# Kernel optimization log

Hardware: AMD Instinct MI355X
Metric: run time of the kernel (lower is better)

The kernel has to match this reference:

```python
import jax, jax.numpy as jnp
import numpy as np

QLEN, BSZ, D_MODEL = 2048, 2, 1024
N_HEAD, D_HEAD = 16, 64
SCALE = 1.0 / (D_HEAD ** 0.5)
LN_EPS = 1e-5


def _rel_shift(x):
    # x: [qlen, klen, bsz, n_head]
    q, k, b, n = x.shape
    zero_pad = jnp.zeros((q, 1, b, n), dtype=x.dtype)
    x_padded = jnp.concatenate([zero_pad, x], axis=1).reshape(k + 1, q, b, n)
    return x_padded[1:].reshape(q, k, b, n)


def setup_inputs() -> dict:
    key = jax.random.key(0)
    ks = jax.random.split(key, 6)
    w = jax.random.normal(ks[0], (QLEN, BSZ, D_MODEL), dtype=jnp.float32)
    r_emb = jax.random.normal(ks[1], (QLEN, N_HEAD, D_HEAD), dtype=jnp.float32) * 0.02
    r_w_bias = jax.random.normal(ks[2], (N_HEAD, D_HEAD), dtype=jnp.float32) * 0.02
    r_bias = jax.random.normal(ks[3], (QLEN, N_HEAD), dtype=jnp.float32) * 0.02
    # causal mask (1 above diagonal => masked), dim==2 branch of original forward
    attn_mask = jnp.triu(jnp.ones((QLEN, QLEN), dtype=jnp.float32), k=1)
    W_qkv = jax.random.normal(ks[4], (D_MODEL, 3 * N_HEAD * D_HEAD), dtype=jnp.float32) * (D_MODEL ** -0.5)
    W_o = jax.random.normal(ks[5], (N_HEAD * D_HEAD, D_MODEL), dtype=jnp.float32) * (D_MODEL ** -0.5)
    ln_g = jnp.ones((D_MODEL,), dtype=jnp.float32)
    ln_b = jnp.zeros((D_MODEL,), dtype=jnp.float32)
    return {"w": w, "r_emb": r_emb, "r_w_bias": r_w_bias, "r_bias": r_bias,
            "attn_mask": attn_mask, "W_qkv": W_qkv, "W_o": W_o, "ln_g": ln_g, "ln_b": ln_b}


def reference(w, r_emb, r_w_bias, r_bias, attn_mask, W_qkv, W_o, ln_g, ln_b):
    qlen, bsz, d_model = w.shape
    n_head, d_head = r_w_bias.shape

    w_heads = w @ W_qkv                                   # [q, b, 3*n*d]
    q_h, k_h, v_h = jnp.split(w_heads, 3, axis=-1)
    q_h = q_h.reshape(qlen, bsz, n_head, d_head)
    k_h = k_h.reshape(qlen, bsz, n_head, d_head)
    v_h = v_h.reshape(qlen, bsz, n_head, d_head)
    klen = k_h.shape[0]

    # klen == r_emb.size(0) here, so slicing is a no-op (kept for fidelity)
    r_emb_s = r_emb[-klen:]
    r_bias_s = r_bias[-klen:]

    rw_head_q = q_h + r_w_bias[None, None]                # [q, b, n, d]
    AC = jnp.einsum('ibnd,jbnd->ijbn', rw_head_q, k_h)    # content-content
    B_ = jnp.einsum('ibnd,jnd->ijbn', q_h, r_emb_s)       # content-position
    D_ = r_bias_s[None, :, None, :]                       # [1, k, 1, n]
    BD = _rel_shift(B_ + D_)

    attn_score = (AC + BD) * SCALE
    attn_score = attn_score + attn_mask[:, :, None, None] * (-1e9)
    attn_prob = jax.nn.softmax(attn_score, axis=1)

    attn_vec = jnp.einsum('ijbn,jbnd->ibnd', attn_prob, v_h)
    attn_vec = attn_vec.reshape(qlen, bsz, n_head * d_head)
    attn_out = attn_vec @ W_o

    # residual + LayerNorm
    y = w + attn_out
    mu = jnp.mean(y, axis=-1, keepdims=True)
    var = jnp.var(y, axis=-1, keepdims=True)
    return (y - mu) / jnp.sqrt(var + LN_EPS) * ln_g + ln_b
```

## Files before the change

kernel.cpp:

```cpp
#include <hip/hip_runtime.h>

typedef unsigned short ushort_t;
typedef unsigned short us4 __attribute__((ext_vector_type(4)));
typedef unsigned short us8 __attribute__((ext_vector_type(8)));
typedef unsigned int   u32x4 __attribute__((ext_vector_type(4)));
typedef float          f32x4 __attribute__((ext_vector_type(4)));
typedef __bf16         bf16x8 __attribute__((ext_vector_type(8)));

#define SCALE2 0.18033688011112042f

__device__ __forceinline__ unsigned short f2bf(float f) {
  unsigned u = __builtin_bit_cast(unsigned, f);
  u += 0x7fffu + ((u >> 16) & 1u);
  return (unsigned short)(u >> 16);
}
__device__ __forceinline__ float bf2f(unsigned short h) {
  unsigned u = ((unsigned)h) << 16;
  return __builtin_bit_cast(float, u);
}

__device__ __forceinline__ float fast_exp2(float x) {
  return __builtin_amdgcn_exp2f(x);
}

__device__ __forceinline__ void async_cp16(const ushort_t* g, ushort_t* l) {
  __builtin_amdgcn_global_load_lds(
      (const __attribute__((address_space(1))) unsigned int*)g,
      (__attribute__((address_space(3))) unsigned int*)l, 16, 0, 0);
}

template <int CTRL>
__device__ __forceinline__ float dpp_rotf(float x) {
  return __builtin_bit_cast(float,
      __builtin_amdgcn_update_dpp(0, __builtin_bit_cast(int, x), CTRL, 0xF, 0xF, true));
}
__device__ __forceinline__ float row16_max(float x) {
  x = fmaxf(x, dpp_rotf<0x121>(x));
  x = fmaxf(x, dpp_rotf<0x122>(x));
  x = fmaxf(x, dpp_rotf<0x124>(x));
  x = fmaxf(x, dpp_rotf<0x128>(x));
  return x;
}
__device__ __forceinline__ float row16_sum(float x) {
  x += dpp_rotf<0x121>(x);
  x += dpp_rotf<0x122>(x);
  x += dpp_rotf<0x124>(x);
  x += dpp_rotf<0x128>(x);
  return x;
}


__global__ __launch_bounds__(256) void k_conv_x(const float* __restrict__ in,
                                                ushort_t* __restrict__ out) {
  int i = (blockIdx.x * 256 + threadIdx.x) * 4;
  float4 v = *(const float4*)(in + i);
  us4 o;
  o[0] = f2bf(v.x); o[1] = f2bf(v.y); o[2] = f2bf(v.z); o[3] = f2bf(v.w);
  *(us4*)(out + i) = o;
}

__global__ __launch_bounds__(256) void k_transpose_bf16(const float* __restrict__ in,
                                                        ushort_t* __restrict__ out,
                                                        int R, int C) {
  __shared__ float tile[32][33];
  int c0 = blockIdx.x * 32, r0 = blockIdx.y * 32;
  int tx = threadIdx.x, ty = threadIdx.y;
#pragma unroll
  for (int k = 0; k < 32; k += 8)
    tile[ty + k][tx] = in[(size_t)(r0 + ty + k) * C + c0 + tx];
  __syncthreads();
#pragma unroll
  for (int k = 0; k < 32; k += 8)
    out[(size_t)(c0 + ty + k) * R + r0 + tx] = f2bf(tile[tx][ty + k]);
}

__global__ __launch_bounds__(256) void k_conv_remb(const float* __restrict__ re,
                                                   ushort_t* __restrict__ out) {
  int tid = blockIdx.x * 256 + threadIdx.x;
  int o = tid * 8;
  int d = o & 63, r = (o >> 6) & 2047, h = o >> 17;
  const float* src = re + ((size_t)r * 16 + h) * 64 + d;
  float4 a = *(const float4*)(src);
  float4 b = *(const float4*)(src + 4);
  us8 u;
  u[0] = f2bf(a.x); u[1] = f2bf(a.y); u[2] = f2bf(a.z); u[3] = f2bf(a.w);
  u[4] = f2bf(b.x); u[5] = f2bf(b.y); u[6] = f2bf(b.z); u[7] = f2bf(b.w);
  *(us8*)(out + o) = u;
}

__global__ __launch_bounds__(256) void k_rbias2(const ushort_t* __restrict__ RE,
                                                const float* __restrict__ rwb,
                                                const float* __restrict__ rbias,
                                                float* __restrict__ out) {
  int tid = blockIdx.x * 256 + threadIdx.x;
  int h = tid >> 11, r = tid & 2047;
  const ushort_t* re = RE + ((size_t)h * 2048 + r) * 64;
  const float* wv = rwb + h * 64;
  float acc = 0.f;
#pragma unroll
  for (int d0 = 0; d0 < 64; d0 += 8) {
    us8 v = *(const us8*)(re + d0);
#pragma unroll
    for (int e = 0; e < 8; ++e) acc += bf2f(v[e]) * wv[d0 + e];
  }
  out[h * 2048 + r] = (rbias[r * 16 + h] - acc) * SCALE2;
}


__global__ __launch_bounds__(256) void k_gemm_qkv(const ushort_t* __restrict__ A,
                                                  const ushort_t* __restrict__ B,
                                                  const float* __restrict__ rwb,
                                                  ushort_t* __restrict__ qt,
                                                  ushort_t* __restrict__ kk,
                                                  ushort_t* __restrict__ vv) {
  __shared__ ushort_t Al[128 * 32], Bl[128 * 32];
  int row0 = blockIdx.x * 128, col0 = blockIdx.y * 128;
  int t = threadIdx.x, w = t >> 6, l = t & 63;
  int wr = w >> 1, wc = w & 1, g = l >> 4, cl = l & 15;
  f32x4 acc[4][4];
#pragma unroll
  for (int m = 0; m < 4; ++m)
#pragma unroll
    for (int n = 0; n < 4; ++n) acc[m][n] = (f32x4){0.f, 0.f, 0.f, 0.f};
  for (int k0 = 0; k0 < 1024; k0 += 32) {
#pragma unroll
    for (int c = 0; c < 2; ++c) {
      int u = t + 256 * c, row = u >> 2, col = (u & 3) * 8;
      async_cp16(A + (size_t)(row0 + row) * 1024 + k0 + col, &Al[u * 8]);
      async_cp16(B + (size_t)(col0 + row) * 1024 + k0 + col, &Bl[u * 8]);
    }
    __syncthreads();
    bf16x8 af[4], bfr[4];
#pragma unroll
    for (int m = 0; m < 4; ++m) af[m] = *(const bf16x8*)(&Al[(wr * 64 + m * 16 + cl) * 32 + g * 8]);
#pragma unroll
    for (int n = 0; n < 4; ++n) bfr[n] = *(const bf16x8*)(&Bl[(wc * 64 + n * 16 + cl) * 32 + g * 8]);
#pragma unroll
    for (int m = 0; m < 4; ++m)
#pragma unroll
      for (int n = 0; n < 4; ++n)
        acc[m][n] = __builtin_amdgcn_mfma_f32_16x16x32_bf16(af[m], bfr[n], acc[m][n], 0, 0, 0);
    __syncthreads();
  }
  int sec = col0 >> 10;
#pragma unroll
  for (int m = 0; m < 4; ++m) {
#pragma unroll
    for (int n = 0; n < 4; ++n) {
#pragma unroll
      for (int r = 0; r < 4; ++r) {
        int row = row0 + wr * 64 + m * 16 + g * 4 + r;
        int col = col0 + wc * 64 + n * 16 + cl;
        int mm = col & 1023, hh = mm >> 6, d = mm & 63;
        int bq = row & 1, iq = row >> 1;
        float val = acc[m][n][r];
        if (sec == 0) {
          qt[(((size_t)bq * 16 + hh) * 2048 + iq) * 64 + d] = f2bf((val + rwb[mm]) * SCALE2);
        } else if (sec == 1) {
          kk[(((size_t)bq * 16 + hh) * 2048 + iq) * 64 + d] = f2bf(val);
        } else {
          vv[(((size_t)bq * 16 + hh) * 64 + d) * 2048 + iq] = f2bf(val);
        }
      }
    }
  }
}


__global__ __launch_bounds__(256, 3) void k_flash(const ushort_t* __restrict__ QT,
                                                  const ushort_t* __restrict__ KK,
                                                  const ushort_t* __restrict__ VT,
                                                  const ushort_t* __restrict__ RE,
                                                  const float* __restrict__ RB2,
                                                  ushort_t* __restrict__ AV) {
  int bh = blockIdx.x, b = bh >> 4, h = bh & 15;
  int i0 = (gridDim.y - 1 - blockIdx.y) * 64;
  int t = threadIdx.x, w = t >> 6, l = t & 63, g = l >> 4, cl = l & 15;

  __shared__ ushort_t Klds[64 * 72];
  __shared__ ushort_t Vt[64 * 72];
  __shared__ ushort_t Rl[128 * 72];
  __shared__ float rb2s[128];
  __shared__ ushort_t Pls[4][16 * 76];
  __shared__ float alphal[4][16];
  __shared__ float lsuml[4][16];

  const ushort_t* qb = QT + ((size_t)(b * 16 + h)) * 2048 * 64;
  const ushort_t* kb = KK + ((size_t)(b * 16 + h)) * 2048 * 64;
  const ushort_t* vt = VT + ((size_t)(b * 16 + h)) * 64 * 2048;
  const ushort_t* rbase = RE + (size_t)h * 2048 * 64;
  const float* r2 = RB2 + h * 2048;

  int qrow = i0 + w * 16 + cl;
  bf16x8 qa0 = *(const bf16x8*)(qb + (size_t)qrow * 64 + g * 8);
  bf16x8 qa1 = *(const bf16x8*)(qb + (size_t)qrow * 64 + 32 + g * 8);

  float m_run[4], l_run[4];
  f32x4 Ot[4];
#pragma unroll
  for (int r = 0; r < 4; ++r) { m_run[r] = -1e30f; l_run[r] = 0.f; }
#pragma unroll
  for (int dt = 0; dt < 4; ++dt) Ot[dt] = (f32x4){0.f, 0.f, 0.f, 0.f};

  int nt = gridDim.y - blockIdx.y;
  int rb0f = 1984 - i0;
  int urow = t >> 3, ucol = (t & 7) * 8;

  *(u32x4*)(&Rl[((rb0f + urow) & 127) * 72 + ucol]) =
      *(const u32x4*)(rbase + (size_t)(rb0f + urow) * 64 + ucol);
  *(u32x4*)(&Rl[((rb0f + urow + 32) & 127) * 72 + ucol]) =
      *(const u32x4*)(rbase + (size_t)(rb0f + urow + 32) * 64 + ucol);
  if (t < 64) rb2s[(rb0f + t) & 127] = r2[rb0f + t];

  u32x4 kreg0, kreg1, vreg0, vreg1, rreg0, rreg1;
  float rb2reg;

  {
    kreg0 = *(const u32x4*)(kb + (size_t)urow * 64 + ucol);
    kreg1 = *(const u32x4*)(kb + (size_t)(urow + 32) * 64 + ucol);
    vreg0 = *(const u32x4*)(vt + (size_t)urow * 2048 + ucol);
    vreg1 = *(const u32x4*)(vt + (size_t)(urow + 32) * 2048 + ucol);
    int gs = rb0f + 64;
    int rr0 = gs + urow, rr1 = gs + urow + 32;
    rreg0 = (rr0 < 2048) ? *(const u32x4*)(rbase + (size_t)rr0 * 64 + ucol) : (u32x4){0u, 0u, 0u, 0u};
    rreg1 = (rr1 < 2048) ? *(const u32x4*)(rbase + (size_t)rr1 * 64 + ucol) : (u32x4){0u, 0u, 0u, 0u};
    int rrb = gs + t;
    rb2reg = (t < 64 && rrb < 2048) ? r2[rrb] : 0.f;
  }

  for (int tt = 0; tt < nt; ++tt) {
    int j0 = tt * 64;
    int rb0 = rb0f + j0;
    __syncthreads();
    {
      *(u32x4*)(&Klds[urow * 72 + ucol]) = kreg0;
      *(u32x4*)(&Klds[(urow + 32) * 72 + ucol]) = kreg1;
      *(u32x4*)(&Vt[urow * 72 + ucol]) = vreg0;
      *(u32x4*)(&Vt[(urow + 32) * 72 + ucol]) = vreg1;
      int gs = rb0 + 64;
      *(u32x4*)(&Rl[((gs + urow) & 127) * 72 + ucol]) = rreg0;
      *(u32x4*)(&Rl[((gs + urow + 32) & 127) * 72 + ucol]) = rreg1;
      if (t < 64) rb2s[(gs + t) & 127] = rb2reg;
    }
    __syncthreads();
    if (tt + 1 < nt) {
      int j0n = j0 + 64;
      kreg0 = *(const u32x4*)(kb + (size_t)(j0n + urow) * 64 + ucol);
      kreg1 = *(const u32x4*)(kb + (size_t)(j0n + urow + 32) * 64 + ucol);
      vreg0 = *(const u32x4*)(vt + (size_t)urow * 2048 + j0n + ucol);
      vreg1 = *(const u32x4*)(vt + (size_t)(urow + 32) * 2048 + j0n + ucol);
      int gs = rb0f + j0n + 64;
      int rr0 = gs + urow, rr1 = gs + urow + 32;
      rreg0 = (rr0 < 2048) ? *(const u32x4*)(rbase + (size_t)rr0 * 64 + ucol) : (u32x4){0u, 0u, 0u, 0u};
      rreg1 = (rr1 < 2048) ? *(const u32x4*)(rbase + (size_t)rr1 * 64 + ucol) : (u32x4){0u, 0u, 0u, 0u};
      int rrb = gs + t;
      rb2reg = (t < 64 && rrb < 2048) ? r2[rrb] : 0.f;
    }

    int bw0 = 48 - 16 * w;
    int rB = rb0 + bw0;
    f32x4 bwf[5];
    __builtin_amdgcn_s_setprio(1);
#pragma unroll
    for (int ct = 0; ct < 5; ++ct) {
      int prow = (rB + ct * 16) & 127;
      f32x4 a = (f32x4){0.f, 0.f, 0.f, 0.f};
      bf16x8 rr0 = *(const bf16x8*)(&Rl[(prow + cl) * 72 + g * 8]);
      a = __builtin_amdgcn_mfma_f32_16x16x32_bf16(qa0, rr0, a, 0, 0, 0);
      bf16x8 rr1 = *(const bf16x8*)(&Rl[(prow + cl) * 72 + 32 + g * 8]);
      a = __builtin_amdgcn_mfma_f32_16x16x32_bf16(qa1, rr1, a, 0, 0, 0);
      float rv = rb2s[(prow + cl) & 127];
      a[0] += rv; a[1] += rv; a[2] += rv; a[3] += rv;
      bwf[ct] = a;
    }

    f32x4 S[4];
#pragma unroll
    for (int ct = 0; ct < 4; ++ct) {
      f32x4 a = (f32x4){0.f, 0.f, 0.f, 0.f};
      bf16x8 kf0 = *(const bf16x8*)(&Klds[(ct * 16 + cl) * 72 + g * 8]);
      a = __builtin_amdgcn_mfma_f32_16x16x32_bf16(qa0, kf0, a, 0, 0, 0);
      bf16x8 kf1 = *(const bf16x8*)(&Klds[(ct * 16 + cl) * 72 + 32 + g * 8]);
      a = __builtin_amdgcn_mfma_f32_16x16x32_bf16(qa1, kf1, a, 0, 0, 0);
      S[ct] = a;
    }
    __builtin_amdgcn_s_setprio(0);

    bool diag = (tt == nt - 1);
    int climit = i0 - j0 + 15 + 16 * w;
#pragma unroll
    for (int r = 0; r < 4; ++r) {
      int rl = g * 4 + r;
      int dlt = cl - rl + 15;
      int src = (l & 48) | (dlt & 15);
      float b0 = __shfl(bwf[0][r], src);
      float b1 = __shfl(bwf[1][r], src);
      float b2 = __shfl(bwf[2][r], src);
      float b3 = __shfl(bwf[3][r], src);
      float b4 = __shfl(bwf[4][r], src);
      if (dlt >= 16) { b0 = b1; b1 = b2; b2 = b3; b3 = b4; }
      float sv[4];
      if (diag) {
        sv[0] = (dlt      <= climit) ? S[0][r] + b0 : -1e30f;
        sv[1] = (dlt + 16 <= climit) ? S[1][r] + b1 : -1e30f;
        sv[2] = (dlt + 32 <= climit) ? S[2][r] + b2 : -1e30f;
        sv[3] = (dlt + 48 <= climit) ? S[3][r] + b3 : -1e30f;
      } else {
        sv[0] = S[0][r] + b0;
        sv[1] = S[1][r] + b1;
        sv[2] = S[2][r] + b2;
        sv[3] = S[3][r] + b3;
      }
      float rmax = fmaxf(fmaxf(sv[0], sv[1]), fmaxf(sv[2], sv[3]));
      rmax = row16_max(rmax);
      float mn = fmaxf(m_run[r], rmax);
      float al = fast_exp2(m_run[r] - mn);
      m_run[r] = mn;
      float rsum = 0.f;
#pragma unroll
      for (int ct = 0; ct < 4; ++ct) {
        float pv = fast_exp2(sv[ct] - mn);
        sv[ct] = pv;
        rsum += pv;
      }
      rsum = row16_sum(rsum);
      l_run[r] = l_run[r] * al + rsum;
      if (cl == 0) alphal[w][rl] = al;
#pragma unroll
      for (int ct = 0; ct < 4; ++ct)
        Pls[w][rl * 76 + ct * 16 + cl] = f2bf(sv[ct]);
    }

    float aq = alphal[w][cl];
    bf16x8 pb0 = *(const bf16x8*)(&Pls[w][cl * 76 + g * 8]);
    bf16x8 pb1 = *(const bf16x8*)(&Pls[w][cl * 76 + 32 + g * 8]);
    __builtin_amdgcn_s_setprio(1);
#pragma unroll
    for (int dt = 0; dt < 4; ++dt) {
      f32x4 o = Ot[dt];
      o[0] *= aq; o[1] *= aq; o[2] *= aq; o[3] *= aq;
      bf16x8 va0 = *(const bf16x8*)(&Vt[(dt * 16 + cl) * 72 + g * 8]);
      o = __builtin_amdgcn_mfma_f32_16x16x32_bf16(va0, pb0, o, 0, 0, 0);
      bf16x8 va1 = *(const bf16x8*)(&Vt[(dt * 16 + cl) * 72 + 32 + g * 8]);
      o = __builtin_amdgcn_mfma_f32_16x16x32_bf16(va1, pb1, o, 0, 0, 0);
      Ot[dt] = o;
    }
    __builtin_amdgcn_s_setprio(0);
  }

  if (cl == 0) {
#pragma unroll
    for (int r = 0; r < 4; ++r) lsuml[w][g * 4 + r] = l_run[r];
  }
  float inv = 1.f / lsuml[w][cl];
  int orow = (i0 + w * 16 + cl) * 2 + b;
#pragma unroll
  for (int dt = 0; dt < 4; ++dt) {
    us4 o4;
    o4[0] = f2bf(Ot[dt][0] * inv);
    o4[1] = f2bf(Ot[dt][1] * inv);
    o4[2] = f2bf(Ot[dt][2] * inv);
    o4[3] = f2bf(Ot[dt][3] * inv);
    *(us4*)(&AV[(size_t)orow * 1024 + h * 64 + dt * 16 + g * 4]) = o4;
  }
}


__global__ __launch_bounds__(256) void k_gemm_o(const ushort_t* __restrict__ A,
                                                const ushort_t* __restrict__ B,
                                                const float* __restrict__ wsrc,
                                                float* __restrict__ Y) {
  __shared__ ushort_t Al[128 * 32], Bl[128 * 32];
  int row0 = blockIdx.x * 128, col0 = blockIdx.y * 128;
  int t = threadIdx.x, w = t >> 6, l = t & 63;
  int wr = w >> 1, wc = w & 1, g = l >> 4, cl = l & 15;
  f32x4 acc[4][4];
#pragma unroll
  for (int m = 0; m < 4; ++m)
#pragma unroll
    for (int n = 0; n < 4; ++n) acc[m][n] = (f32x4){0.f, 0.f, 0.f, 0.f};
  for (int k0 = 0; k0 < 1024; k0 += 32) {
#pragma unroll
    for (int c = 0; c < 2; ++c) {
      int u = t + 256 * c, row = u >> 2, col = (u & 3) * 8;
      async_cp16(A + (size_t)(row0 + row) * 1024 + k0 + col, &Al[u * 8]);
      async_cp16(B + (size_t)(col0 + row) * 1024 + k0 + col, &Bl[u * 8]);
    }
    __syncthreads();
    bf16x8 af[4], bfr[4];
#pragma unroll
    for (int m = 0; m < 4; ++m) af[m] = *(const bf16x8*)(&Al[(wr * 64 + m * 16 + cl) * 32 + g * 8]);
#pragma unroll
    for (int n = 0; n < 4; ++n) bfr[n] = *(const bf16x8*)(&Bl[(wc * 64 + n * 16 + cl) * 32 + g * 8]);
#pragma unroll
    for (int m = 0; m < 4; ++m)
#pragma unroll
      for (int n = 0; n < 4; ++n)
        acc[m][n] = __builtin_amdgcn_mfma_f32_16x16x32_bf16(af[m], bfr[n], acc[m][n], 0, 0, 0);
    __syncthreads();
  }
#pragma unroll
  for (int m = 0; m < 4; ++m) {
#pragma unroll
    for (int n = 0; n < 4; ++n) {
#pragma unroll
      for (int r = 0; r < 4; ++r) {
        int row = row0 + wr * 64 + m * 16 + g * 4 + r;
        int col = col0 + wc * 64 + n * 16 + cl;
        size_t idx = (size_t)row * 1024 + col;
        Y[idx] = acc[m][n][r] + wsrc[idx];
      }
    }
  }
}


__global__ __launch_bounds__(256) void k_ln(const float* __restrict__ Y,
                                            const float* __restrict__ gg,
                                            const float* __restrict__ bb,
                                            float* __restrict__ out) {
  int row = blockIdx.x, t = threadIdx.x;
  float4 v = *(const float4*)(Y + (size_t)row * 1024 + t * 4);
  float s = v.x + v.y + v.z + v.w;
  float q = v.x * v.x + v.y * v.y + v.z * v.z + v.w * v.w;
#pragma unroll
  for (int m = 32; m >= 1; m >>= 1) {
    s += __shfl_xor(s, m);
    q += __shfl_xor(q, m);
  }
  __shared__ float ssh[4], qsh[4];
  int w = t >> 6, l = t & 63;
  if (l == 0) { ssh[w] = s; qsh[w] = q; }
  __syncthreads();
  s = ssh[0] + ssh[1] + ssh[2] + ssh[3];
  q = qsh[0] + qsh[1] + qsh[2] + qsh[3];
  float mu = s * (1.f / 1024.f);
  float var = q * (1.f / 1024.f) - mu * mu;
  float rstd = rsqrtf(var + 1e-5f);
  float4 gv = *(const float4*)(gg + t * 4);
  float4 bv = *(const float4*)(bb + t * 4);
  float4 o;
  o.x = (v.x - mu) * rstd * gv.x + bv.x;
  o.y = (v.y - mu) * rstd * gv.y + bv.y;
  o.z = (v.z - mu) * rstd * gv.z + bv.z;
  o.w = (v.w - mu) * rstd * gv.w + bv.w;
  *(float4*)(out + (size_t)row * 1024 + t * 4) = o;
}


extern "C" void kernel_launch(void* const* d_in, const int* in_sizes, int n_in,
                              void* d_out, int out_size, void* d_ws, size_t ws_size,
                              hipStream_t stream) {
  const float* w      = (const float*)d_in[0];
  const float* r_emb  = (const float*)d_in[1];
  const float* r_w_b  = (const float*)d_in[2];
  const float* r_bias = (const float*)d_in[3];
  const float* W_qkv  = (const float*)d_in[5];
  const float* W_o    = (const float*)d_in[6];
  const float* ln_g   = (const float*)d_in[7];
  const float* ln_b   = (const float*)d_in[8];
  float* out = (float*)d_out;
  char* ws = (char*)d_ws;

  ushort_t* X16  = (ushort_t*)(ws + 0);
  ushort_t* WQ16 = (ushort_t*)(ws + 8388608);
  ushort_t* WO16 = (ushort_t*)(ws + 14680064);
  ushort_t* RE16 = (ushort_t*)(ws + 16777216);
  float*    RB2  = (float*)(ws + 20971520);
  ushort_t* QT16 = (ushort_t*)(ws + 21102592);
  ushort_t* K16  = (ushort_t*)(ws + 29491200);
  ushort_t* VT16 = (ushort_t*)(ws + 37879808);
  ushort_t* AV16 = (ushort_t*)(ws + 46268416);
  float*    Y32  = (float*)(ws + 54657024);

  k_conv_x<<<4096, 256, 0, stream>>>(w, X16);
  k_transpose_bf16<<<dim3(96, 32), dim3(32, 8), 0, stream>>>(W_qkv, WQ16, 1024, 3072);
  k_transpose_bf16<<<dim3(32, 32), dim3(32, 8), 0, stream>>>(W_o, WO16, 1024, 1024);
  k_conv_remb<<<1024, 256, 0, stream>>>(r_emb, RE16);
  k_rbias2<<<128, 256, 0, stream>>>(RE16, r_w_b, r_bias, RB2);
  k_gemm_qkv<<<dim3(32, 24), 256, 0, stream>>>(X16, WQ16, r_w_b, QT16, K16, VT16);
  k_flash<<<dim3(32, 32), 256, 0, stream>>>(QT16, K16, VT16, RE16, RB2, AV16);
  k_gemm_o<<<dim3(32, 8), 256, 0, stream>>>(AV16, WO16, w, Y32);
  k_ln<<<4096, 256, 0, stream>>>(Y32, ln_g, ln_b, out);
}
```

Baseline: 171.6 us.

## Stage V transpose through LDS and store residual pre-LN buffer in bf16

Result: slower. 178.8 us (+4.2%).

```diff
diff --git a/kernel.cpp b/kernel.cpp
--- a/kernel.cpp
+++ b/kernel.cpp
@@ -113,7 +113,9 @@
                                                   ushort_t* __restrict__ qt,
                                                   ushort_t* __restrict__ kk,
                                                   ushort_t* __restrict__ vv) {
-  __shared__ ushort_t Al[128 * 32], Bl[128 * 32];
+  __shared__ ushort_t SM[9216];
+  ushort_t* Al = SM;
+  ushort_t* Bl = SM + 4096;
   int row0 = blockIdx.x * 128, col0 = blockIdx.y * 128;
   int t = threadIdx.x, w = t >> 6, l = t & 63;
   int wr = w >> 1, wc = w & 1, g = l >> 4, cl = l & 15;
@@ -143,24 +145,51 @@
     __syncthreads();
   }
   int sec = col0 >> 10;
-#pragma unroll
-  for (int m = 0; m < 4; ++m) {
-#pragma unroll
-    for (int n = 0; n < 4; ++n) {
-#pragma unroll
-      for (int r = 0; r < 4; ++r) {
-        int row = row0 + wr * 64 + m * 16 + g * 4 + r;
-        int col = col0 + wc * 64 + n * 16 + cl;
-        int mm = col & 1023, hh = mm >> 6, d = mm & 63;
-        int bq = row & 1, iq = row >> 1;
-        float val = acc[m][n][r];
-        if (sec == 0) {
-          qt[(((size_t)bq * 16 + hh) * 2048 + iq) * 64 + d] = f2bf((val + rwb[mm]) * SCALE2);
-        } else if (sec == 1) {
-          kk[(((size_t)bq * 16 + hh) * 2048 + iq) * 64 + d] = f2bf(val);
-        } else {
-          vv[(((size_t)bq * 16 + hh) * 64 + d) * 2048 + iq] = f2bf(val);
+  if (sec != 2) {
+#pragma unroll
+    for (int m = 0; m < 4; ++m) {
+#pragma unroll
+      for (int n = 0; n < 4; ++n) {
+#pragma unroll
+        for (int r = 0; r < 4; ++r) {
+          int row = row0 + wr * 64 + m * 16 + g * 4 + r;
+          int col = col0 + wc * 64 + n * 16 + cl;
+          int mm = col & 1023, hh = mm >> 6, d = mm & 63;
+          int bq = row & 1, iq = row >> 1;
+          float val = acc[m][n][r];
+          if (sec == 0) {
+            qt[(((size_t)bq * 16 + hh) * 2048 + iq) * 64 + d] = f2bf((val + rwb[mm]) * SCALE2);
+          } else {
+            kk[(((size_t)bq * 16 + hh) * 2048 + iq) * 64 + d] = f2bf(val);
+          }
         }
+      }
+    }
+  } else {
+    int hh0 = (col0 & 1023) >> 6;
+    int iq0 = row0 >> 1;
+#pragma unroll
+    for (int bq = 0; bq < 2; ++bq) {
+      __syncthreads();
+#pragma unroll
+      for (int m = 0; m < 4; ++m)
+#pragma unroll
+        for (int n = 0; n < 4; ++n)
+#pragma unroll
+          for (int rr = 0; rr < 2; ++rr) {
+            int r = bq + rr * 2;
+            int row_local = wr * 64 + m * 16 + g * 4 + r;
+            int iql = row_local >> 1;
+            int dd = n * 16 + cl;
+            SM[wc * 4608 + dd * 72 + iql] = f2bf(acc[m][n][r]);
+          }
+      __syncthreads();
+#pragma unroll
+      for (int it = 0; it < 4; ++it) {
+        int u = t + 256 * it;
+        int pan = u >> 9, dd = (u >> 3) & 63, grp = u & 7;
+        us8 vvv = *(const us8*)(&SM[pan * 4608 + dd * 72 + grp * 8]);
+        *(us8*)(&vv[(((size_t)bq * 16 + hh0 + pan) * 64 + dd) * 2048 + iq0 + grp * 8]) = vvv;
       }
     }
   }
@@ -368,8 +397,8 @@
 
 __global__ __launch_bounds__(256) void k_gemm_o(const ushort_t* __restrict__ A,
                                                 const ushort_t* __restrict__ B,
-                                                const float* __restrict__ wsrc,
-                                                float* __restrict__ Y) {
+                                                const ushort_t* __restrict__ wsrc,
+                                                ushort_t* __restrict__ Y) {
   __shared__ ushort_t Al[128 * 32], Bl[128 * 32];
   int row0 = blockIdx.x * 128, col0 = blockIdx.y * 128;
   int t = threadIdx.x, w = t >> 6, l = t & 63;
@@ -408,21 +437,22 @@
         int row = row0 + wr * 64 + m * 16 + g * 4 + r;
         int col = col0 + wc * 64 + n * 16 + cl;
         size_t idx = (size_t)row * 1024 + col;
-        Y[idx] = acc[m][n][r] + wsrc[idx];
+        Y[idx] = f2bf(acc[m][n][r] + bf2f(wsrc[idx]));
       }
     }
   }
 }
 
 
-__global__ __launch_bounds__(256) void k_ln(const float* __restrict__ Y,
+__global__ __launch_bounds__(256) void k_ln(const ushort_t* __restrict__ Y,
                                             const float* __restrict__ gg,
                                             const float* __restrict__ bb,
                                             float* __restrict__ out) {
   int row = blockIdx.x, t = threadIdx.x;
-  float4 v = *(const float4*)(Y + (size_t)row * 1024 + t * 4);
-  float s = v.x + v.y + v.z + v.w;
-  float q = v.x * v.x + v.y * v.y + v.z * v.z + v.w * v.w;
+  us4 yv = *(const us4*)(Y + (size_t)row * 1024 + t * 4);
+  float v0 = bf2f(yv[0]), v1 = bf2f(yv[1]), v2 = bf2f(yv[2]), v3 = bf2f(yv[3]);
+  float s = v0 + v1 + v2 + v3;
+  float q = v0 * v0 + v1 * v1 + v2 * v2 + v3 * v3;
 #pragma unroll
   for (int m = 32; m >= 1; m >>= 1) {
     s += __shfl_xor(s, m);
@@ -440,10 +470,10 @@
   float4 gv = *(const float4*)(gg + t * 4);
   float4 bv = *(const float4*)(bb + t * 4);
   float4 o;
-  o.x = (v.x - mu) * rstd * gv.x + bv.x;
-  o.y = (v.y - mu) * rstd * gv.y + bv.y;
-  o.z = (v.z - mu) * rstd * gv.z + bv.z;
-  o.w = (v.w - mu) * rstd * gv.w + bv.w;
+  o.x = (v0 - mu) * rstd * gv.x + bv.x;
+  o.y = (v1 - mu) * rstd * gv.y + bv.y;
+  o.z = (v2 - mu) * rstd * gv.z + bv.z;
+  o.w = (v3 - mu) * rstd * gv.w + bv.w;
   *(float4*)(out + (size_t)row * 1024 + t * 4) = o;
 }
 
@@ -471,7 +501,7 @@
   ushort_t* K16  = (ushort_t*)(ws + 29491200);
   ushort_t* VT16 = (ushort_t*)(ws + 37879808);
   ushort_t* AV16 = (ushort_t*)(ws + 46268416);
-  float*    Y32  = (float*)(ws + 54657024);
+  ushort_t* Y16  = (ushort_t*)(ws + 54657024);
 
   k_conv_x<<<4096, 256, 0, stream>>>(w, X16);
   k_transpose_bf16<<<dim3(96, 32), dim3(32, 8), 0, stream>>>(W_qkv, WQ16, 1024, 3072);
@@ -480,6 +510,6 @@
   k_rbias2<<<128, 256, 0, stream>>>(RE16, r_w_b, r_bias, RB2);
   k_gemm_qkv<<<dim3(32, 24), 256, 0, stream>>>(X16, WQ16, r_w_b, QT16, K16, VT16);
   k_flash<<<dim3(32, 32), 256, 0, stream>>>(QT16, K16, VT16, RE16, RB2, AV16);
-  k_gemm_o<<<dim3(32, 8), 256, 0, stream>>>(AV16, WO16, w, Y32);
-  k_ln<<<4096, 256, 0, stream>>>(Y32, ln_g, ln_b, out);
-}
+  k_gemm_o<<<dim3(32, 8), 256, 0, stream>>>(AV16, WO16, X16, Y16);
+  k_ln<<<4096, 256, 0, stream>>>(Y16, ln_g, ln_b, out);
+}
```
